# Optimization experiments

Hardware: AMD Instinct MI355X
Metric: run time of the kernel (lower is better)

The kernel has to match this reference:

```python
import jax, jax.numpy as jnp
import numpy as np

N_EMBD = 1024
N_HEAD = 16
T_LEN = 4096
BATCH = 1


def setup_inputs() -> dict:
    key = jax.random.key(0)
    ks = jax.random.split(key, 9)
    C = N_EMBD
    s = 1.0 / np.sqrt(C)
    inp = {
        "x": jax.random.normal(ks[0], (BATCH, T_LEN, C), dtype=jnp.float32),
        "wq": jax.random.normal(ks[1], (C, C), dtype=jnp.float32) * s,
        "bq": jax.random.normal(ks[2], (C,), dtype=jnp.float32) * s,
        "wk": jax.random.normal(ks[3], (C, C), dtype=jnp.float32) * s,
        "bk": jax.random.normal(ks[4], (C,), dtype=jnp.float32) * s,
        "wv": jax.random.normal(ks[5], (C, C), dtype=jnp.float32) * s,
        "bv": jax.random.normal(ks[6], (C,), dtype=jnp.float32) * s,
        "wp": jax.random.normal(ks[7], (C, C), dtype=jnp.float32) * s,
        "bp": jax.random.normal(ks[8], (C,), dtype=jnp.float32) * s,
    }
    return inp


def reference(x, wq, bq, wk, bk, wv, bv, wp, bp):
    B, T, C = x.shape
    H = N_HEAD
    D = C // H  # head_dim
    # torch nn.Linear: y = x @ W.T + b
    def lin(x, w, b):
        return jnp.einsum("btc,oc->bto", x, w) + b
    q = lin(x, wq, bq).reshape(B, T, H, D).transpose(0, 2, 1, 3)  # bhtd
    k = lin(x, wk, bk).reshape(B, T, H, D).transpose(0, 2, 1, 3)
    v = lin(x, wv, bv).reshape(B, T, H, D).transpose(0, 2, 1, 3)
    att = jnp.einsum("bhqd,bhkd->bhqk", q, k) / jnp.sqrt(jnp.float32(D))
    causal = jnp.tril(jnp.ones((T, T), dtype=bool))  # [T,T]
    att = jnp.where(causal[None, None, :, :], att, -jnp.inf)
    att = jax.nn.softmax(att, axis=-1)
    # dropout p=0.0 -> identity (eval equivalent)
    y = jnp.einsum("bhqk,bhkd->bhqd", att, v)
    y = y.transpose(0, 2, 1, 3).reshape(B, T, C)
    return jnp.einsum("btc,oc->bto", y, wp) + bp
```

## Files before the change

kernel.cpp:

```cpp
#include <hip/hip_runtime.h>
#include <stdint.h>

#define T_LEN 4096
#define C_DIM 1024
#define NH 16
#define CLOG2E 0.18033688011112042f

typedef uint16_t u16;
typedef __attribute__((ext_vector_type(4))) float f32x4;
typedef __attribute__((ext_vector_type(8))) __bf16 bf16x8;
typedef __attribute__((ext_vector_type(8))) uint16_t u16x8;
typedef __attribute__((ext_vector_type(4))) float fvec4;

static __device__ __forceinline__ u16 f2b(float f) {
  union { float f; uint32_t u; } v; v.f = f;
  uint32_t u = v.u;
  return (u16)((u + 0x7fffu + ((u >> 16) & 1u)) >> 16);
}

static __device__ __forceinline__ uint32_t cvtpk(float lo, float hi) {
  uint32_t r;
  asm("v_cvt_pk_bf16_f32 %0, %1, %2" : "=v"(r) : "v"(lo), "v"(hi));
  return r;
}

static __device__ __forceinline__ f32x4 mfma16(u16x8 a, u16x8 b, f32x4 c) {
  return __builtin_amdgcn_mfma_f32_16x16x32_bf16(
      __builtin_bit_cast(bf16x8, a), __builtin_bit_cast(bf16x8, b), c, 0, 0, 0);
}

static __device__ __forceinline__ void gload_lds16(const void* g, void* l) {
  __builtin_amdgcn_global_load_lds(
      (const __attribute__((address_space(1))) uint32_t*)g,
      (__attribute__((address_space(3))) uint32_t*)l, 16, 0, 0);
}

__global__ void cvt_kernel(const float* __restrict__ in, u16* __restrict__ out, int n8) {
  int i = blockIdx.x * blockDim.x + threadIdx.x;
  if (i >= n8) return;
  const fvec4* p = (const fvec4*)(in + (size_t)i * 8);
  fvec4 a = p[0], b = p[1];
  u16x8 o;
  o[0] = f2b(a[0]); o[1] = f2b(a[1]); o[2] = f2b(a[2]); o[3] = f2b(a[3]);
  o[4] = f2b(b[0]); o[5] = f2b(b[1]); o[6] = f2b(b[2]); o[7] = f2b(b[3]);
  *(u16x8*)(out + (size_t)i * 8) = o;
}

__global__ void wcvt_kernel(const float* __restrict__ w0, const float* __restrict__ w1,
                            const float* __restrict__ w2, const float* __restrict__ w3,
                            u16* __restrict__ o0, u16* __restrict__ o1,
                            u16* __restrict__ o2, u16* __restrict__ o3, int n8) {
  int i = blockIdx.x * blockDim.x + threadIdx.x;
  if (i >= n8) return;
  const int z = blockIdx.y;
  const float* in = (z == 0) ? w0 : (z == 1) ? w1 : (z == 2) ? w2 : w3;
  u16* out = (z == 0) ? o0 : (z == 1) ? o1 : (z == 2) ? o2 : o3;
  const fvec4* p = (const fvec4*)(in + (size_t)i * 8);
  fvec4 a = p[0], b = p[1];
  u16x8 o;
  o[0] = f2b(a[0]); o[1] = f2b(a[1]); o[2] = f2b(a[2]); o[3] = f2b(a[3]);
  o[4] = f2b(b[0]); o[5] = f2b(b[1]); o[6] = f2b(b[2]); o[7] = f2b(b[3]);
  *(u16x8*)(out + (size_t)i * 8) = o;
}

__global__ __launch_bounds__(256) void gemm_qkv(
    const u16* __restrict__ xb,
    const u16* __restrict__ wqb, const u16* __restrict__ wkb, const u16* __restrict__ wvb,
    const float* __restrict__ bq, const float* __restrict__ bk, const float* __restrict__ bv,
    u16* __restrict__ qh, u16* __restrict__ kh, u16* __restrict__ vt)
{
  __shared__ u16 sA[128 * 32];
  __shared__ u16 sB[128 * 32];
  const int K = C_DIM;
  const int z = blockIdx.z;
  const u16* wb = (z == 0) ? wqb : (z == 1) ? wkb : wvb;
  const float* bias = (z == 0) ? bq : (z == 1) ? bk : bv;
  const int m0 = blockIdx.x * 128;
  const int n0 = blockIdx.y * 128;
  const int tid = threadIdx.x;
  const int lane = tid & 63;
  const int w = tid >> 6;
  const int wm = (w >> 1) * 64;
  const int wn = (w & 1) * 64;
  const int lr = lane & 15;
  const int lk = (lane >> 4) * 8;

  f32x4 acc[4][4];
#pragma unroll
  for (int m = 0; m < 4; ++m)
#pragma unroll
    for (int n = 0; n < 4; ++n) acc[m][n] = (f32x4){0.f, 0.f, 0.f, 0.f};

  const int srow = tid >> 2;
  const int scol = (tid & 3) * 8;
  const u16* gA = xb + (size_t)(m0 + srow) * K + scol;
  const u16* gB = wb + (size_t)(n0 + srow) * K + scol;

  for (int k0 = 0; k0 < K; k0 += 32) {
    gload_lds16(gA + k0,          &sA[tid * 8]);
    gload_lds16(gA + 64 * K + k0, &sA[2048 + tid * 8]);
    gload_lds16(gB + k0,          &sB[tid * 8]);
    gload_lds16(gB + 64 * K + k0, &sB[2048 + tid * 8]);
    __syncthreads();
    u16x8 af[4], bfr[4];
#pragma unroll
    for (int m = 0; m < 4; ++m) af[m]  = *(const u16x8*)&sA[(wm + m * 16 + lr) * 32 + lk];
#pragma unroll
    for (int n = 0; n < 4; ++n) bfr[n] = *(const u16x8*)&sB[(wn + n * 16 + lr) * 32 + lk];
#pragma unroll
    for (int m = 0; m < 4; ++m)
#pragma unroll
      for (int n = 0; n < 4; ++n) acc[m][n] = mfma16(af[m], bfr[n], acc[m][n]);
    __syncthreads();
  }

  const int lg = lane >> 4;
#pragma unroll
  for (int n = 0; n < 4; ++n) {
    const int o = n0 + wn + n * 16 + lr;
    const float bb = bias[o];
    const int h = o >> 6;
    const int d = o & 63;
#pragma unroll
    for (int m = 0; m < 4; ++m) {
      const int tb = m0 + wm + m * 16 + lg * 4;
      if (z == 2) {
        uint2 pk;
        pk.x = cvtpk(acc[m][n][0] + bb, acc[m][n][1] + bb);
        pk.y = cvtpk(acc[m][n][2] + bb, acc[m][n][3] + bb);
        *(uint2*)&vt[(size_t)o * T_LEN + tb] = pk;
      } else if (z == 0) {
#pragma unroll
        for (int r = 0; r < 4; ++r)
          qh[((size_t)h * T_LEN + tb + r) * 64 + d] = f2b((acc[m][n][r] + bb) * CLOG2E);
      } else {
#pragma unroll
        for (int r = 0; r < 4; ++r)
          kh[((size_t)h * T_LEN + tb + r) * 64 + d] = f2b(acc[m][n][r] + bb);
      }
    }
  }
}

__global__ __launch_bounds__(256) void gemm_proj(
    const u16* __restrict__ yb, const u16* __restrict__ wpb,
    const float* __restrict__ bp, float* __restrict__ out)
{
  __shared__ u16 sA[128 * 32];
  __shared__ u16 sB[128 * 32];
  const int K = C_DIM;
  const int m0 = blockIdx.x * 128;
  const int n0 = blockIdx.y * 128;
  const int tid = threadIdx.x;
  const int lane = tid & 63;
  const int w = tid >> 6;
  const int wm = (w >> 1) * 64;
  const int wn = (w & 1) * 64;
  const int lr = lane & 15;
  const int lk = (lane >> 4) * 8;

  f32x4 acc[4][4];
#pragma unroll
  for (int m = 0; m < 4; ++m)
#pragma unroll
    for (int n = 0; n < 4; ++n) acc[m][n] = (f32x4){0.f, 0.f, 0.f, 0.f};

  const int srow = tid >> 2;
  const int scol = (tid & 3) * 8;
  const u16* gA = yb  + (size_t)(m0 + srow) * K + scol;
  const u16* gB = wpb + (size_t)(n0 + srow) * K + scol;

  for (int k0 = 0; k0 < K; k0 += 32) {
    gload_lds16(gA + k0,          &sA[tid * 8]);
    gload_lds16(gA + 64 * K + k0, &sA[2048 + tid * 8]);
    gload_lds16(gB + k0,          &sB[tid * 8]);
    gload_lds16(gB + 64 * K + k0, &sB[2048 + tid * 8]);
    __syncthreads();
    u16x8 af[4], bfr[4];
#pragma unroll
    for (int m = 0; m < 4; ++m) af[m]  = *(const u16x8*)&sA[(wm + m * 16 + lr) * 32 + lk];
#pragma unroll
    for (int n = 0; n < 4; ++n) bfr[n] = *(const u16x8*)&sB[(wn + n * 16 + lr) * 32 + lk];
#pragma unroll
    for (int m = 0; m < 4; ++m)
#pragma unroll
      for (int n = 0; n < 4; ++n) acc[m][n] = mfma16(af[m], bfr[n], acc[m][n]);
    __syncthreads();
  }

  const int lg = lane >> 4;
#pragma unroll
  for (int n = 0; n < 4; ++n) {
    const int o = n0 + wn + n * 16 + lr;
    const float bb = bp[o];
#pragma unroll
    for (int m = 0; m < 4; ++m) {
      const int tb = m0 + wm + m * 16 + lg * 4;
#pragma unroll
      for (int r = 0; r < 4; ++r)
        out[(size_t)(tb + r) * C_DIM + o] = acc[m][n][r] + bb;
    }
  }
}

__global__ __launch_bounds__(256) void attn_kernel(
    const u16* __restrict__ qh, const u16* __restrict__ kh, const u16* __restrict__ vt,
    u16* __restrict__ y)
{
  __shared__ char skb[2][8192];
  __shared__ char svb[2][8192];
  __shared__ u16 pp[4][16][64];
  const int bid = blockIdx.x;
  const int j = bid >> 3;
  const int h = ((bid & 7) << 1) + (j & 1);
  const int qb = 63 - (j >> 1);
  const int nt = qb + 1;
  const int tid = threadIdx.x;
  const int lane = tid & 63;
  const int w = tid >> 6;
  const int lr = lane & 15;
  const int lg = lane >> 4;
  const int sw = (lr & 7) << 4;
  const int qt0 = qb * 64 + w * 16;

  const int srow = tid >> 2;
  const int scb = (tid & 3) * 32;
  const int wo0 = srow * 128 + (scb ^ ((srow & 7) << 4));
  const int wo1 = srow * 128 + ((scb + 16) ^ ((srow & 7) << 4));
  const u16* gkbase = kh + ((size_t)h * T_LEN + srow) * 64 + (tid & 3) * 16;
  const u16* gvbase = vt + ((size_t)h * 64 + srow) * T_LEN + (tid & 3) * 16;
  char* ppb = (char*)&pp[w][0][0];

  const u16* qbase = qh + ((size_t)h * T_LEN + qt0 + lr) * 64 + lg * 8;
  u16x8 qf0 = *(const u16x8*)(qbase);
  u16x8 qf1 = *(const u16x8*)(qbase + 32);

  f32x4 oacc[4];
#pragma unroll
  for (int i = 0; i < 4; ++i) oacc[i] = (f32x4){0.f, 0.f, 0.f, 0.f};
  float mrow = -1e30f, lsum = 0.f;

  u16x8 ka = *(const u16x8*)(gkbase);
  u16x8 kb = *(const u16x8*)(gkbase + 8);
  u16x8 va = *(const u16x8*)(gvbase);
  u16x8 vb = *(const u16x8*)(gvbase + 8);
  *(u16x8*)(skb[0] + wo0) = ka; *(u16x8*)(skb[0] + wo1) = kb;
  *(u16x8*)(svb[0] + wo0) = va; *(u16x8*)(svb[0] + wo1) = vb;
  int cur = 0;

  for (int t = 0; t < nt; ++t) {
    __syncthreads();
    if (t + 1 < nt) {
      const size_t ko = (size_t)(t + 1) * 4096;
      ka = *(const u16x8*)(gkbase + ko);
      kb = *(const u16x8*)(gkbase + ko + 8);
      va = *(const u16x8*)(gvbase + (t + 1) * 64);
      vb = *(const u16x8*)(gvbase + (t + 1) * 64 + 8);
    }
    const char* skc = skb[cur];
    const char* svc = svb[cur];

    f32x4 sacc[4];
    __builtin_amdgcn_s_setprio(1);
#pragma unroll
    for (int i = 0; i < 4; ++i) {
      const int ro = (i * 16 + lr) * 128;
      u16x8 a0 = *(const u16x8*)(skc + ro + ((lg * 16) ^ sw));
      u16x8 a1 = *(const u16x8*)(skc + ro + ((lg * 16 + 64) ^ sw));
      f32x4 zz = (f32x4){0.f, 0.f, 0.f, 0.f};
      zz = mfma16(a0, qf0, zz);
      zz = mfma16(a1, qf1, zz);
      sacc[i] = zz;
    }
    __builtin_amdgcn_s_setprio(0);

    float pvv[4][4];
    float pm = -1e30f;
    if (t == nt - 1) {
      const int qg = qt0 + lr;
      const int kt0 = t * 64;
#pragma unroll
      for (int i = 0; i < 4; ++i) {
#pragma unroll
        for (int r = 0; r < 4; ++r) {
          const int kt = kt0 + i * 16 + lg * 4 + r;
          pvv[i][r] = (kt <= qg) ? sacc[i][r] : -1e30f;
        }
        pm = fmaxf(pm, fmaxf(fmaxf(pvv[i][0], pvv[i][1]), fmaxf(pvv[i][2], pvv[i][3])));
      }
    } else {
#pragma unroll
      for (int i = 0; i < 4; ++i) {
#pragma unroll
        for (int r = 0; r < 4; ++r) pvv[i][r] = sacc[i][r];
        pm = fmaxf(pm, fmaxf(fmaxf(pvv[i][0], pvv[i][1]), fmaxf(pvv[i][2], pvv[i][3])));
      }
    }

    if (!__all(pm <= mrow)) {
      float pmf = fmaxf(pm, __shfl_xor(pm, 16));
      pmf = fmaxf(pmf, __shfl_xor(pmf, 32));
      const float mnew = fmaxf(mrow, pmf);
      const float sc = exp2f(mrow - mnew);
      lsum *= sc;
#pragma unroll
      for (int i = 0; i < 4; ++i) oacc[i] *= sc;
      mrow = mnew;
    }

    float tsum = 0.f;
#pragma unroll
    for (int i = 0; i < 4; ++i) {
      float e0 = exp2f(pvv[i][0] - mrow);
      float e1 = exp2f(pvv[i][1] - mrow);
      float e2 = exp2f(pvv[i][2] - mrow);
      float e3 = exp2f(pvv[i][3] - mrow);
      tsum += (e0 + e1) + (e2 + e3);
      uint2 pk;
      pk.x = cvtpk(e0, e1);
      pk.y = cvtpk(e2, e3);
      *(uint2*)(ppb + ((lr * 128 + i * 32 + lg * 8) ^ sw)) = pk;
    }
    lsum += tsum;

    __builtin_amdgcn_s_setprio(1);
#pragma unroll
    for (int ks = 0; ks < 2; ++ks) {
      u16x8 pf = *(const u16x8*)(ppb + ((lr * 128 + lg * 16 + ks * 64) ^ sw));
#pragma unroll
      for (int dblk = 0; dblk < 4; ++dblk) {
        const int ro = (dblk * 16 + lr) * 128;
        u16x8 vf = *(const u16x8*)(svc + ro + ((lg * 16 + ks * 64) ^ sw));
        oacc[dblk] = mfma16(vf, pf, oacc[dblk]);
      }
    }
    __builtin_amdgcn_s_setprio(0);

    if (t + 1 < nt) {
      char* dk = skb[cur ^ 1];
      char* dv = svb[cur ^ 1];
      *(u16x8*)(dk + wo0) = ka; *(u16x8*)(dk + wo1) = kb;
      *(u16x8*)(dv + wo0) = va; *(u16x8*)(dv + wo1) = vb;
    }
    cur ^= 1;
  }

  lsum += __shfl_xor(lsum, 16);
  lsum += __shfl_xor(lsum, 32);
  const float inv = 1.0f / lsum;
#pragma unroll
  for (int dblk = 0; dblk < 4; ++dblk) {
    uint2 pk;
    pk.x = cvtpk(oacc[dblk][0] * inv, oacc[dblk][1] * inv);
    pk.y = cvtpk(oacc[dblk][2] * inv, oacc[dblk][3] * inv);
    *(uint2*)&y[(size_t)(qt0 + lr) * C_DIM + h * 64 + dblk * 16 + lg * 4] = pk;
  }
}

extern "C" void kernel_launch(void* const* d_in, const int* in_sizes, int n_in,
                              void* d_out, int out_size, void* d_ws, size_t ws_size,
                              hipStream_t stream) {
  const float* x  = (const float*)d_in[0];
  const float* wq = (const float*)d_in[1];
  const float* bq = (const float*)d_in[2];
  const float* wk = (const float*)d_in[3];
  const float* bk = (const float*)d_in[4];
  const float* wv = (const float*)d_in[5];
  const float* bv = (const float*)d_in[6];
  const float* wp = (const float*)d_in[7];
  const float* bp = (const float*)d_in[8];

  char* ws = (char*)d_ws;
  const size_t MB = 1024 * 1024;
  u16* xb  = (u16*)(ws + 0 * MB);
  u16* wqb = (u16*)(ws + 8 * MB);
  u16* wkb = (u16*)(ws + 10 * MB);
  u16* wvb = (u16*)(ws + 12 * MB);
  u16* wpb = (u16*)(ws + 14 * MB);
  u16* qh  = (u16*)(ws + 16 * MB);
  u16* kh  = (u16*)(ws + 24 * MB);
  u16* vt  = (u16*)(ws + 32 * MB);
  u16* y   = (u16*)(ws + 40 * MB);

  cvt_kernel<<<dim3(2048), dim3(256), 0, stream>>>(x, xb, 524288);
  wcvt_kernel<<<dim3(512, 4), dim3(256), 0, stream>>>(
      wq, wk, wv, wp, wqb, wkb, wvb, wpb, 131072);

  gemm_qkv<<<dim3(32, 8, 3), dim3(256), 0, stream>>>(
      xb, wqb, wkb, wvb, bq, bk, bv, qh, kh, vt);

  attn_kernel<<<dim3(1024), dim3(256), 0, stream>>>(qh, kh, vt, y);

  gemm_proj<<<dim3(32, 8), dim3(256), 0, stream>>>(y, wpb, bp, (float*)d_out);
}
```

Baseline: 153.3 us.

## Merge cast kernels, shrink proj GEMM tile, streamline softmax max/sum

Combines the x and weight fp32-to-bf16 conversion kernels into a single launch, removing one kernel launch. Changes the output projection GEMM tile from 128x128 to 128x64, which doubles the grid to 512 blocks for better occupancy on the many CUs. In attention, masking is done in place on the score registers, the row max uses a flatter reduction tree and the exp sum uses four independent accumulators to shorten dependency chains. The smaller proj tile lowers data reuse per block.

Measured after the change: 147.1 us. -4.0%, faster.

```diff
diff --git a/kernel.cpp b/kernel.cpp
--- a/kernel.cpp
+++ b/kernel.cpp
@@ -35,26 +35,24 @@
       (__attribute__((address_space(3))) uint32_t*)l, 16, 0, 0);
 }
 
-__global__ void cvt_kernel(const float* __restrict__ in, u16* __restrict__ out, int n8) {
+__global__ void cast_all(const float* __restrict__ x,
+                         const float* __restrict__ wq, const float* __restrict__ wk,
+                         const float* __restrict__ wv, const float* __restrict__ wp,
+                         u16* __restrict__ xb,
+                         u16* __restrict__ wqb, u16* __restrict__ wkb,
+                         u16* __restrict__ wvb, u16* __restrict__ wpb) {
   int i = blockIdx.x * blockDim.x + threadIdx.x;
-  if (i >= n8) return;
-  const fvec4* p = (const fvec4*)(in + (size_t)i * 8);
-  fvec4 a = p[0], b = p[1];
-  u16x8 o;
-  o[0] = f2b(a[0]); o[1] = f2b(a[1]); o[2] = f2b(a[2]); o[3] = f2b(a[3]);
-  o[4] = f2b(b[0]); o[5] = f2b(b[1]); o[6] = f2b(b[2]); o[7] = f2b(b[3]);
-  *(u16x8*)(out + (size_t)i * 8) = o;
-}
-
-__global__ void wcvt_kernel(const float* __restrict__ w0, const float* __restrict__ w1,
-                            const float* __restrict__ w2, const float* __restrict__ w3,
-                            u16* __restrict__ o0, u16* __restrict__ o1,
-                            u16* __restrict__ o2, u16* __restrict__ o3, int n8) {
-  int i = blockIdx.x * blockDim.x + threadIdx.x;
-  if (i >= n8) return;
+  if (i >= 131072) return;
   const int z = blockIdx.y;
-  const float* in = (z == 0) ? w0 : (z == 1) ? w1 : (z == 2) ? w2 : w3;
-  u16* out = (z == 0) ? o0 : (z == 1) ? o1 : (z == 2) ? o2 : o3;
+  const float* in;
+  u16* out;
+  if (z < 4) {
+    in  = (z == 0) ? wq  : (z == 1) ? wk  : (z == 2) ? wv  : wp;
+    out = (z == 0) ? wqb : (z == 1) ? wkb : (z == 2) ? wvb : wpb;
+  } else {
+    in  = x  + (size_t)(z - 4) * 131072 * 8;
+    out = xb + (size_t)(z - 4) * 131072 * 8;
+  }
   const fvec4* p = (const fvec4*)(in + (size_t)i * 8);
   fvec4 a = p[0], b = p[1];
   u16x8 o;
@@ -147,21 +145,20 @@
     const float* __restrict__ bp, float* __restrict__ out)
 {
   __shared__ u16 sA[128 * 32];
-  __shared__ u16 sB[128 * 32];
+  __shared__ u16 sB[64 * 32];
   const int K = C_DIM;
   const int m0 = blockIdx.x * 128;
-  const int n0 = blockIdx.y * 128;
+  const int n0 = blockIdx.y * 64;
   const int tid = threadIdx.x;
   const int lane = tid & 63;
   const int w = tid >> 6;
-  const int wm = (w >> 1) * 64;
-  const int wn = (w & 1) * 64;
+  const int wm = w * 32;
   const int lr = lane & 15;
   const int lk = (lane >> 4) * 8;
 
-  f32x4 acc[4][4];
-#pragma unroll
-  for (int m = 0; m < 4; ++m)
+  f32x4 acc[2][4];
+#pragma unroll
+  for (int m = 0; m < 2; ++m)
 #pragma unroll
     for (int n = 0; n < 4; ++n) acc[m][n] = (f32x4){0.f, 0.f, 0.f, 0.f};
 
@@ -174,15 +171,14 @@
     gload_lds16(gA + k0,          &sA[tid * 8]);
     gload_lds16(gA + 64 * K + k0, &sA[2048 + tid * 8]);
     gload_lds16(gB + k0,          &sB[tid * 8]);
-    gload_lds16(gB + 64 * K + k0, &sB[2048 + tid * 8]);
-    __syncthreads();
-    u16x8 af[4], bfr[4];
-#pragma unroll
-    for (int m = 0; m < 4; ++m) af[m]  = *(const u16x8*)&sA[(wm + m * 16 + lr) * 32 + lk];
-#pragma unroll
-    for (int n = 0; n < 4; ++n) bfr[n] = *(const u16x8*)&sB[(wn + n * 16 + lr) * 32 + lk];
-#pragma unroll
-    for (int m = 0; m < 4; ++m)
+    __syncthreads();
+    u16x8 af[2], bfr[4];
+#pragma unroll
+    for (int m = 0; m < 2; ++m) af[m]  = *(const u16x8*)&sA[(wm + m * 16 + lr) * 32 + lk];
+#pragma unroll
+    for (int n = 0; n < 4; ++n) bfr[n] = *(const u16x8*)&sB[(n * 16 + lr) * 32 + lk];
+#pragma unroll
+    for (int m = 0; m < 2; ++m)
 #pragma unroll
       for (int n = 0; n < 4; ++n) acc[m][n] = mfma16(af[m], bfr[n], acc[m][n]);
     __syncthreads();
@@ -191,10 +187,10 @@
   const int lg = lane >> 4;
 #pragma unroll
   for (int n = 0; n < 4; ++n) {
-    const int o = n0 + wn + n * 16 + lr;
+    const int o = n0 + n * 16 + lr;
     const float bb = bp[o];
 #pragma unroll
-    for (int m = 0; m < 4; ++m) {
+    for (int m = 0; m < 2; ++m) {
       const int tb = m0 + wm + m * 16 + lg * 4;
 #pragma unroll
       for (int r = 0; r < 4; ++r)
@@ -274,28 +270,23 @@
     }
     __builtin_amdgcn_s_setprio(0);
 
-    float pvv[4][4];
-    float pm = -1e30f;
     if (t == nt - 1) {
       const int qg = qt0 + lr;
       const int kt0 = t * 64;
 #pragma unroll
-      for (int i = 0; i < 4; ++i) {
+      for (int i = 0; i < 4; ++i)
 #pragma unroll
         for (int r = 0; r < 4; ++r) {
           const int kt = kt0 + i * 16 + lg * 4 + r;
-          pvv[i][r] = (kt <= qg) ? sacc[i][r] : -1e30f;
+          sacc[i][r] = (kt <= qg) ? sacc[i][r] : -1e30f;
         }
-        pm = fmaxf(pm, fmaxf(fmaxf(pvv[i][0], pvv[i][1]), fmaxf(pvv[i][2], pvv[i][3])));
-      }
-    } else {
-#pragma unroll
-      for (int i = 0; i < 4; ++i) {
-#pragma unroll
-        for (int r = 0; r < 4; ++r) pvv[i][r] = sacc[i][r];
-        pm = fmaxf(pm, fmaxf(fmaxf(pvv[i][0], pvv[i][1]), fmaxf(pvv[i][2], pvv[i][3])));
-      }
-    }
+    }
+    float x0 = fmaxf(fmaxf(sacc[0][0], sacc[0][1]), sacc[0][2]);
+    float x1 = fmaxf(fmaxf(sacc[0][3], sacc[1][0]), sacc[1][1]);
+    float x2 = fmaxf(fmaxf(sacc[1][2], sacc[1][3]), sacc[2][0]);
+    float x3 = fmaxf(fmaxf(sacc[2][1], sacc[2][2]), sacc[2][3]);
+    float x4 = fmaxf(fmaxf(sacc[3][0], sacc[3][1]), sacc[3][2]);
+    float pm = fmaxf(fmaxf(fmaxf(x0, x1), fmaxf(x2, x3)), fmaxf(x4, sacc[3][3]));
 
     if (!__all(pm <= mrow)) {
       float pmf = fmaxf(pm, __shfl_xor(pm, 16));
@@ -308,20 +299,20 @@
       mrow = mnew;
     }
 
-    float tsum = 0.f;
+    float t0 = 0.f, t1 = 0.f, t2 = 0.f, t3 = 0.f;
 #pragma unroll
     for (int i = 0; i < 4; ++i) {
-      float e0 = exp2f(pvv[i][0] - mrow);
-      float e1 = exp2f(pvv[i][1] - mrow);
-      float e2 = exp2f(pvv[i][2] - mrow);
-      float e3 = exp2f(pvv[i][3] - mrow);
-      tsum += (e0 + e1) + (e2 + e3);
+      float e0 = exp2f(sacc[i][0] - mrow);
+      float e1 = exp2f(sacc[i][1] - mrow);
+      float e2 = exp2f(sacc[i][2] - mrow);
+      float e3 = exp2f(sacc[i][3] - mrow);
+      t0 += e0; t1 += e1; t2 += e2; t3 += e3;
       uint2 pk;
       pk.x = cvtpk(e0, e1);
       pk.y = cvtpk(e2, e3);
       *(uint2*)(ppb + ((lr * 128 + i * 32 + lg * 8) ^ sw)) = pk;
     }
-    lsum += tsum;
+    lsum += (t0 + t1) + (t2 + t3);
 
     __builtin_amdgcn_s_setprio(1);
 #pragma unroll
@@ -382,14 +373,13 @@
   u16* vt  = (u16*)(ws + 32 * MB);
   u16* y   = (u16*)(ws + 40 * MB);
 
-  cvt_kernel<<<dim3(2048), dim3(256), 0, stream>>>(x, xb, 524288);
-  wcvt_kernel<<<dim3(512, 4), dim3(256), 0, stream>>>(
-      wq, wk, wv, wp, wqb, wkb, wvb, wpb, 131072);
+  cast_all<<<dim3(512, 8), dim3(256), 0, stream>>>(
+      x, wq, wk, wv, wp, xb, wqb, wkb, wvb, wpb);
 
   gemm_qkv<<<dim3(32, 8, 3), dim3(256), 0, stream>>>(
       xb, wqb, wkb, wvb, bq, bk, bv, qh, kh, vt);
 
   attn_kernel<<<dim3(1024), dim3(256), 0, stream>>>(qh, kh, vt, y);
 
-  gemm_proj<<<dim3(32, 8), dim3(256), 0, stream>>>(y, wpb, bp, (float*)d_out);
-}
+  gemm_proj<<<dim3(32, 16), dim3(256), 0, stream>>>(y, wpb, bp, (float*)d_out);
+}
```
